# Kernel optimization log

Hardware: AMD Instinct MI355X
Metric: run time of the kernel (lower is better)

Reference implementation:

```python
import jax, jax.numpy as jnp
import numpy as np

EMBED_DIM = 768
NUM_HEADS = 12
HEAD_SIZE = EMBED_DIM // NUM_HEADS


def setup_inputs() -> dict:
    key = jax.random.key(0)
    ks = jax.random.split(key, 9)
    B, S, D = 4, 2048, EMBED_DIM
    scale = 1.0 / np.sqrt(D)
    x = jax.random.normal(ks[0], (B, S, D), dtype=jnp.float32)
    # Linear params (torch nn.Linear: y = x @ W.T + b); store W as [in, out] for einsum
    Wq = jax.random.normal(ks[1], (D, D), dtype=jnp.float32) * scale
    bq = jnp.zeros((D,), dtype=jnp.float32)
    Wk = jax.random.normal(ks[2], (D, D), dtype=jnp.float32) * scale
    bk = jnp.zeros((D,), dtype=jnp.float32)
    Wv = jax.random.normal(ks[3], (D, D), dtype=jnp.float32) * scale
    bv = jnp.zeros((D,), dtype=jnp.float32)
    Wo = jax.random.normal(ks[4], (D, D), dtype=jnp.float32) * scale
    bo = jnp.zeros((D,), dtype=jnp.float32)
    return {"x": x, "Wq": Wq, "bq": bq, "Wk": Wk, "bk": bk,
            "Wv": Wv, "bv": bv, "Wo": Wo, "bo": bo}


def reference(x, Wq, bq, Wk, bk, Wv, bv, Wo, bo):
    B, S, D = x.shape
    H, hs = NUM_HEADS, HEAD_SIZE
    scale = hs ** (-0.5)
    # Projections
    Q = (x @ Wq + bq).reshape(B, S, H, hs)
    K = (x @ Wk + bk).reshape(B, S, H, hs)
    V = (x @ Wv + bv).reshape(B, S, H, hs)
    # Batched attention over all heads (equivalent to the per-head loop:
    # torch view splits last dim into H contiguous chunks; concat of per-head
    # outputs along -1 restores the same layout)
    scores = jnp.einsum('bqhd,bkhd->bhqk', Q, K) * scale  # [B,H,S,S]
    attn = jax.nn.softmax(scores, axis=-1)
    out = jnp.einsum('bhqk,bkhd->bqhd', attn, V).reshape(B, S, D)
    # Output projection; dropout is identity in eval mode
    return out @ Wo + bo
```

## Files before the change

kernel.cpp:

```cpp
#include <hip/hip_runtime.h>

typedef unsigned short ushort_t;
typedef __bf16 bf16x8 __attribute__((ext_vector_type(8)));
typedef float floatx4 __attribute__((ext_vector_type(4)));

__device__ inline ushort_t f2bf(float f) {
    __bf16 h = (__bf16)f;
    return __builtin_bit_cast(ushort_t, h);
}

__device__ inline void gload16(const void* g, void* l) {
    __builtin_amdgcn_global_load_lds((const __attribute__((address_space(1))) void*)g,
                                     (__attribute__((address_space(3))) void*)l, 16, 0, 0);
}

__global__ __launch_bounds__(256) void prep_kernel(
    const float* __restrict__ x, ushort_t* __restrict__ xbf,
    const float* __restrict__ W0, const float* __restrict__ W1,
    const float* __restrict__ W2, const float* __restrict__ W3,
    ushort_t* __restrict__ T0, ushort_t* __restrict__ T1,
    ushort_t* __restrict__ T2, ushort_t* __restrict__ T3) {
    int bx = blockIdx.x;
    int tid = threadIdx.x;
    if (bx < 2304) {
        __shared__ float t[32][33];
        int w = bx / 576, rem = bx % 576;
        const float* W; ushort_t* T;
        switch (w) {
            case 0: W = W0; T = T0; break;
            case 1: W = W1; T = T1; break;
            case 2: W = W2; T = T2; break;
            default: W = W3; T = T3; break;
        }
        int n0 = (rem / 24) * 32, k0 = (rem % 24) * 32;
        int tx = tid & 31, ty = tid >> 5;
        for (int i = 0; i < 4; ++i)
            t[ty + i * 8][tx] = W[(k0 + ty + i * 8) * 768 + n0 + tx];
        __syncthreads();
        for (int i = 0; i < 4; ++i)
            T[(n0 + ty + i * 8) * 768 + k0 + tx] = f2bf(t[tx][ty + i * 8]);
    } else {
        int i = ((bx - 2304) * 256 + tid) * 4;
        float4 v = *(const float4*)(x + i);
        ushort4 u;
        u.x = f2bf(v.x); u.y = f2bf(v.y); u.z = f2bf(v.z); u.w = f2bf(v.w);
        *(ushort4*)(xbf + i) = u;
    }
}

__global__ __launch_bounds__(256) void gemm_qkv(
    const ushort_t* __restrict__ A,
    const ushort_t* __restrict__ Tq, const ushort_t* __restrict__ Tk, const ushort_t* __restrict__ Tv,
    const float* __restrict__ bq, const float* __restrict__ bk, const float* __restrict__ bv,
    ushort_t* __restrict__ Qb, ushort_t* __restrict__ Kb, ushort_t* __restrict__ Vtb) {
    __shared__ ushort_t As[128 * 64];
    __shared__ ushort_t Bs[64 * 64];
    int tid = threadIdx.x;
    int m0 = blockIdx.x * 128;
    int by = blockIdx.y;
    int which = by / 12;
    int n0 = (by % 12) * 64;
    const ushort_t* Bt = which == 0 ? Tq : (which == 1 ? Tk : Tv);
    const float* bias = which == 0 ? bq : (which == 1 ? bk : bv);

    int wave = tid >> 6;
    int lane = tid & 63;
    int ln = tid & 15;
    int quad = (tid >> 4) & 3;
    int wm = wave * 32;
    int lr = lane >> 3;
    int lc = (lane & 7) * 8;

    floatx4 acc[2][4];
    floatx4 z = {0.f, 0.f, 0.f, 0.f};
    for (int i = 0; i < 2; ++i)
        for (int j = 0; j < 4; ++j) acc[i][j] = z;

    for (int kt = 0; kt < 12; ++kt) {
        int k0 = kt * 64;
        __syncthreads();
        for (int i = 0; i < 4; ++i) {
            int c = wave * 4 + i;
            gload16(&A[(m0 + c * 8 + lr) * 768 + k0 + lc], &As[c * 512]);
        }
        for (int i = 0; i < 2; ++i) {
            int c = wave * 2 + i;
            gload16(&Bt[(n0 + c * 8 + lr) * 768 + k0 + lc], &Bs[c * 512]);
        }
        __syncthreads();
        for (int ks = 0; ks < 2; ++ks) {
            bf16x8 a[2], b[4];
            for (int i = 0; i < 2; ++i)
                a[i] = *(const bf16x8*)&As[(wm + i * 16 + ln) * 64 + ks * 32 + quad * 8];
            for (int j = 0; j < 4; ++j)
                b[j] = *(const bf16x8*)&Bs[(j * 16 + ln) * 64 + ks * 32 + quad * 8];
            for (int i = 0; i < 2; ++i)
                for (int j = 0; j < 4; ++j)
                    acc[i][j] = __builtin_amdgcn_mfma_f32_16x16x32_bf16(a[i], b[j], acc[i][j], 0, 0, 0);
        }
    }

    const float QSCALE = 0.125f * 1.44269504088896f;
    for (int i = 0; i < 2; ++i) {
        for (int j = 0; j < 4; ++j) {
            int gn = n0 + j * 16 + ln;
            float bia = bias[gn];
            int h = gn >> 6, dd = gn & 63;
            for (int r = 0; r < 4; ++r) {
                int gm = m0 + wm + i * 16 + quad * 4 + r;
                int bb = gm >> 11, ss = gm & 2047;
                float v = acc[i][j][r] + bia;
                if (which == 0) {
                    Qb[((bb * 12 + h) * 2048 + ss) * 64 + dd] = f2bf(v * QSCALE);
                } else if (which == 1) {
                    Kb[((bb * 12 + h) * 2048 + ss) * 64 + dd] = f2bf(v);
                } else {
                    Vtb[((bb * 12 + h) * 64 + dd) * 2048 + ss] = f2bf(v);
                }
            }
        }
    }
}

__global__ __launch_bounds__(256) void attn_kernel(
    const ushort_t* __restrict__ Qb, const ushort_t* __restrict__ Kb,
    const ushort_t* __restrict__ Vtb, ushort_t* __restrict__ Ob) {
    __shared__ ushort_t Ks[2][64 * 72];
    __shared__ ushort_t Vs[2][64 * 72];
    int tid = threadIdx.x;
    int qt = blockIdx.x;
    int bh = blockIdx.y;
    int wave = tid >> 6;
    int ln = tid & 15;
    int quad = (tid >> 4) & 3;
    int q0 = qt * 128 + wave * 32;

    const ushort_t* Qp = Qb + (size_t)bh * 2048 * 64;
    const ushort_t* Kp = Kb + (size_t)bh * 2048 * 64;
    const ushort_t* Vp = Vtb + (size_t)bh * 64 * 2048;

    bf16x8 bqf[2][2];
    for (int g = 0; g < 2; ++g)
        for (int ks = 0; ks < 2; ++ks)
            bqf[g][ks] = *(const bf16x8*)&Qp[(q0 + g * 16 + ln) * 64 + ks * 32 + quad * 8];

    int srow = tid >> 3;
    int c8 = tid & 7;
    int scol = c8 * 8;
    int u = c8 & 3;
    int vcol = (c8 >> 2) * 32 + (u & 1) * 16 + (u >> 1) * 4;

    uint4 kreg[2], vreg[2];

    for (int p = 0; p < 2; ++p) {
        kreg[p] = *(const uint4*)&Kp[(p * 32 + srow) * 64 + scol];
        vreg[p] = *(const uint4*)&Vp[(p * 32 + srow) * 2048 + scol];
    }
    for (int p = 0; p < 2; ++p) {
        *(uint4*)&Ks[0][(p * 32 + srow) * 72 + scol] = kreg[p];
        ushort_t* vb = &Vs[0][(p * 32 + srow) * 72 + vcol];
        *(uint2*)vb = make_uint2(vreg[p].x, vreg[p].y);
        *(uint2*)(vb + 8) = make_uint2(vreg[p].z, vreg[p].w);
    }
    __syncthreads();

    floatx4 o_acc[2][4];
    float lsum[2] = {0.f, 0.f};
    floatx4 z = {0.f, 0.f, 0.f, 0.f};
    for (int g = 0; g < 2; ++g)
        for (int m4 = 0; m4 < 4; ++m4) o_acc[g][m4] = z;

    for (int kt = 0; kt < 32; ++kt) {
        int cur = kt & 1;
        if (kt < 31) {
            for (int p = 0; p < 2; ++p) {
                kreg[p] = *(const uint4*)&Kp[((kt + 1) * 64 + p * 32 + srow) * 64 + scol];
                vreg[p] = *(const uint4*)&Vp[(p * 32 + srow) * 2048 + (kt + 1) * 64 + scol];
            }
        }

        const ushort_t* KsH = Ks[cur];
        const ushort_t* VsH = Vs[cur];

        bf16x8 ak[4][2];
        for (int m4 = 0; m4 < 4; ++m4)
            for (int ks = 0; ks < 2; ++ks)
                ak[m4][ks] = *(const bf16x8*)&KsH[(m4 * 16 + ln) * 72 + ks * 32 + quad * 8];

        floatx4 st[2][4];
        for (int g = 0; g < 2; ++g)
            for (int m4 = 0; m4 < 4; ++m4) {
                floatx4 s = z;
                s = __builtin_amdgcn_mfma_f32_16x16x32_bf16(ak[m4][0], bqf[g][0], s, 0, 0, 0);
                s = __builtin_amdgcn_mfma_f32_16x16x32_bf16(ak[m4][1], bqf[g][1], s, 0, 0, 0);
                st[g][m4] = s;
            }

        float pv[2][4][4];
        for (int g = 0; g < 2; ++g)
            for (int m4 = 0; m4 < 4; ++m4)
                for (int r = 0; r < 4; ++r) {
                    float e = __builtin_amdgcn_exp2f(st[g][m4][r]);
                    pv[g][m4][r] = e;
                    lsum[g] += e;
                }

        bf16x8 av[4][2];
        for (int m4 = 0; m4 < 4; ++m4)
            for (int c = 0; c < 2; ++c)
                av[m4][c] = *(const bf16x8*)&VsH[(m4 * 16 + ln) * 72 + c * 32 + quad * 8];

        for (int g = 0; g < 2; ++g) {
            bf16x8 bp[2];
            for (int c = 0; c < 2; ++c) {
                bf16x8 b;
                b[0] = (__bf16)pv[g][2 * c][0];
                b[1] = (__bf16)pv[g][2 * c][1];
                b[2] = (__bf16)pv[g][2 * c][2];
                b[3] = (__bf16)pv[g][2 * c][3];
                b[4] = (__bf16)pv[g][2 * c + 1][0];
                b[5] = (__bf16)pv[g][2 * c + 1][1];
                b[6] = (__bf16)pv[g][2 * c + 1][2];
                b[7] = (__bf16)pv[g][2 * c + 1][3];
                bp[c] = b;
            }
            for (int m4 = 0; m4 < 4; ++m4)
                for (int c = 0; c < 2; ++c)
                    o_acc[g][m4] = __builtin_amdgcn_mfma_f32_16x16x32_bf16(av[m4][c], bp[c], o_acc[g][m4], 0, 0, 0);
        }

        if (kt < 31) {
            int nxt = cur ^ 1;
            for (int p = 0; p < 2; ++p) {
                *(uint4*)&Ks[nxt][(p * 32 + srow) * 72 + scol] = kreg[p];
                ushort_t* vb = &Vs[nxt][(p * 32 + srow) * 72 + vcol];
                *(uint2*)vb = make_uint2(vreg[p].x, vreg[p].y);
                *(uint2*)(vb + 8) = make_uint2(vreg[p].z, vreg[p].w);
            }
        }
        __syncthreads();
    }

    for (int g = 0; g < 2; ++g) {
        lsum[g] += __shfl_xor(lsum[g], 16);
        lsum[g] += __shfl_xor(lsum[g], 32);
    }

    int b = bh / 12, h = bh % 12;
    for (int g = 0; g < 2; ++g) {
        float inv = 1.f / lsum[g];
        int token = b * 2048 + q0 + g * 16 + ln;
        for (int m4 = 0; m4 < 4; ++m4)
            for (int r = 0; r < 4; ++r)
                Ob[token * 768 + h * 64 + m4 * 16 + quad * 4 + r] = f2bf(o_acc[g][m4][r] * inv);
    }
}

__global__ __launch_bounds__(256) void gemm_out(
    const ushort_t* __restrict__ A, const ushort_t* __restrict__ Bt,
    const float* __restrict__ bias, float* __restrict__ out) {
    __shared__ ushort_t As[64 * 64];
    __shared__ ushort_t Bs[64 * 64];
    int tid = threadIdx.x;
    int m0 = blockIdx.x * 64;
    int n0 = blockIdx.y * 64;

    int wave = tid >> 6;
    int lane = tid & 63;
    int ln = tid & 15;
    int quad = (tid >> 4) & 3;
    int lr = lane >> 3;
    int lc = (lane & 7) * 8;

    floatx4 acc[4];
    floatx4 z = {0.f, 0.f, 0.f, 0.f};
    for (int i = 0; i < 4; ++i) acc[i] = z;

    for (int kt = 0; kt < 12; ++kt) {
        int k0 = kt * 64;
        __syncthreads();
        for (int i = 0; i < 2; ++i) {
            int c = wave * 2 + i;
            gload16(&A[(m0 + c * 8 + lr) * 768 + k0 + lc], &As[c * 512]);
            gload16(&Bt[(n0 + c * 8 + lr) * 768 + k0 + lc], &Bs[c * 512]);
        }
        __syncthreads();
        for (int ks = 0; ks < 2; ++ks) {
            bf16x8 b = *(const bf16x8*)&Bs[(wave * 16 + ln) * 64 + ks * 32 + quad * 8];
            for (int i = 0; i < 4; ++i) {
                bf16x8 a = *(const bf16x8*)&As[(i * 16 + ln) * 64 + ks * 32 + quad * 8];
                acc[i] = __builtin_amdgcn_mfma_f32_16x16x32_bf16(a, b, acc[i], 0, 0, 0);
            }
        }
    }

    int gn = n0 + wave * 16 + ln;
    float bia = bias[gn];
    for (int i = 0; i < 4; ++i) {
        for (int r = 0; r < 4; ++r) {
            int gm = m0 + i * 16 + quad * 4 + r;
            out[gm * 768 + gn] = acc[i][r] + bia;
        }
    }
}

extern "C" void kernel_launch(void* const* d_in, const int* in_sizes, int n_in,
                              void* d_out, int out_size, void* d_ws, size_t ws_size,
                              hipStream_t stream) {
    const float* x  = (const float*)d_in[0];
    const float* Wq = (const float*)d_in[1];
    const float* bq = (const float*)d_in[2];
    const float* Wk = (const float*)d_in[3];
    const float* bk = (const float*)d_in[4];
    const float* Wv = (const float*)d_in[5];
    const float* bv = (const float*)d_in[6];
    const float* Wo = (const float*)d_in[7];
    const float* bo = (const float*)d_in[8];

    const int NTOK = 4 * 2048;
    const int NELT = NTOK * 768;
    const int WELT = 768 * 768;

    ushort_t* xbf = (ushort_t*)d_ws;
    ushort_t* Tq  = xbf + NELT;
    ushort_t* Tk  = Tq + WELT;
    ushort_t* Tv  = Tk + WELT;
    ushort_t* To  = Tv + WELT;
    ushort_t* Qb  = To + WELT;
    ushort_t* Kb  = Qb + NELT;
    ushort_t* Vtb = Kb + NELT;
    ushort_t* Ob  = Vtb + NELT;

    prep_kernel<<<8448, 256, 0, stream>>>(x, xbf, Wq, Wk, Wv, Wo, Tq, Tk, Tv, To);
    gemm_qkv<<<dim3(64, 36), 256, 0, stream>>>(xbf, Tq, Tk, Tv, bq, bk, bv, Qb, Kb, Vtb);
    attn_kernel<<<dim3(16, 48), 256, 0, stream>>>(Qb, Kb, Vtb, Ob);
    gemm_out<<<dim3(128, 12), 256, 0, stream>>>(Ob, To, bo, (float*)d_out);
}
```

Before: 232.2 us.

## Stage V transpose through LDS and compute softmax row sums with MFMA

The V projection epilogue now writes its tile transposed into shared memory and then emits coalesced 16-byte stores to the transposed V buffer, instead of scattered 2-byte strided global stores. In the attention kernel, the per-row exponential sum is computed by an extra MFMA against a vector of ones using the bf16-rounded probabilities, replacing scalar adds and cross-lane shuffles. This removes VALU work and keeps the normaliser consistent with the bf16 P used for PV, at the cost of two extra MFMAs per tile per group and an added barrier plus LDS round trip in the V epilogue.

```diff
diff --git a/kernel.cpp b/kernel.cpp
--- a/kernel.cpp
+++ b/kernel.cpp
@@ -53,8 +53,9 @@
     const ushort_t* __restrict__ Tq, const ushort_t* __restrict__ Tk, const ushort_t* __restrict__ Tv,
     const float* __restrict__ bq, const float* __restrict__ bk, const float* __restrict__ bv,
     ushort_t* __restrict__ Qb, ushort_t* __restrict__ Kb, ushort_t* __restrict__ Vtb) {
-    __shared__ ushort_t As[128 * 64];
-    __shared__ ushort_t Bs[64 * 64];
+    __shared__ ushort_t sh[128 * 64 + 64 * 64];
+    ushort_t* As = sh;
+    ushort_t* Bs = sh + 128 * 64;
     int tid = threadIdx.x;
     int m0 = blockIdx.x * 128;
     int by = blockIdx.y;
@@ -101,23 +102,47 @@
     }
 
     const float QSCALE = 0.125f * 1.44269504088896f;
-    for (int i = 0; i < 2; ++i) {
+    if (which != 2) {
+        for (int i = 0; i < 2; ++i) {
+            for (int j = 0; j < 4; ++j) {
+                int gn = n0 + j * 16 + ln;
+                float bia = bias[gn];
+                int h = gn >> 6, dd = gn & 63;
+                for (int r = 0; r < 4; ++r) {
+                    int gm = m0 + wm + i * 16 + quad * 4 + r;
+                    int bb = gm >> 11, ss = gm & 2047;
+                    float v = acc[i][j][r] + bia;
+                    if (which == 0) {
+                        Qb[((bb * 12 + h) * 2048 + ss) * 64 + dd] = f2bf(v * QSCALE);
+                    } else {
+                        Kb[((bb * 12 + h) * 2048 + ss) * 64 + dd] = f2bf(v);
+                    }
+                }
+            }
+        }
+    } else {
+        __syncthreads();
+        ushort_t* tr = sh;
         for (int j = 0; j < 4; ++j) {
-            int gn = n0 + j * 16 + ln;
-            float bia = bias[gn];
-            int h = gn >> 6, dd = gn & 63;
-            for (int r = 0; r < 4; ++r) {
-                int gm = m0 + wm + i * 16 + quad * 4 + r;
-                int bb = gm >> 11, ss = gm & 2047;
-                float v = acc[i][j][r] + bia;
-                if (which == 0) {
-                    Qb[((bb * 12 + h) * 2048 + ss) * 64 + dd] = f2bf(v * QSCALE);
-                } else if (which == 1) {
-                    Kb[((bb * 12 + h) * 2048 + ss) * 64 + dd] = f2bf(v);
-                } else {
-                    Vtb[((bb * 12 + h) * 64 + dd) * 2048 + ss] = f2bf(v);
-                }
-            }
+            int nl = j * 16 + ln;
+            float bia = bias[n0 + nl];
+            for (int i = 0; i < 2; ++i) {
+                ushort4 u;
+                u.x = f2bf(acc[i][j][0] + bia);
+                u.y = f2bf(acc[i][j][1] + bia);
+                u.z = f2bf(acc[i][j][2] + bia);
+                u.w = f2bf(acc[i][j][3] + bia);
+                *(ushort4*)&tr[nl * 136 + wm + i * 16 + quad * 4] = u;
+            }
+        }
+        __syncthreads();
+        int bb = m0 >> 11, ss0 = m0 & 2047;
+        int head = by % 12;
+        for (int p = 0; p < 4; ++p) {
+            int n = p * 16 + (tid >> 4);
+            int mc = (tid & 15) * 8;
+            uint4 v = *(const uint4*)&tr[n * 136 + mc];
+            *(uint4*)&Vtb[(size_t)((bb * 12 + head) * 64 + n) * 2048 + ss0 + mc] = v;
         }
     }
 }
@@ -144,6 +169,9 @@
         for (int ks = 0; ks < 2; ++ks)
             bqf[g][ks] = *(const bf16x8*)&Qp[(q0 + g * 16 + ln) * 64 + ks * 32 + quad * 8];
 
+    bf16x8 ones;
+    for (int k = 0; k < 8; ++k) ones[k] = (__bf16)1.0f;
+
     int srow = tid >> 3;
     int c8 = tid & 7;
     int scol = c8 * 8;
@@ -165,10 +193,12 @@
     __syncthreads();
 
     floatx4 o_acc[2][4];
-    float lsum[2] = {0.f, 0.f};
+    floatx4 s_acc[2];
     floatx4 z = {0.f, 0.f, 0.f, 0.f};
-    for (int g = 0; g < 2; ++g)
+    for (int g = 0; g < 2; ++g) {
+        s_acc[g] = z;
         for (int m4 = 0; m4 < 4; ++m4) o_acc[g][m4] = z;
+    }
 
     for (int kt = 0; kt < 32; ++kt) {
         int cur = kt & 1;
@@ -199,11 +229,8 @@
         float pv[2][4][4];
         for (int g = 0; g < 2; ++g)
             for (int m4 = 0; m4 < 4; ++m4)
-                for (int r = 0; r < 4; ++r) {
-                    float e = __builtin_amdgcn_exp2f(st[g][m4][r]);
-                    pv[g][m4][r] = e;
-                    lsum[g] += e;
-                }
+                for (int r = 0; r < 4; ++r)
+                    pv[g][m4][r] = __builtin_amdgcn_exp2f(st[g][m4][r]);
 
         bf16x8 av[4][2];
         for (int m4 = 0; m4 < 4; ++m4)
@@ -227,6 +254,8 @@
             for (int m4 = 0; m4 < 4; ++m4)
                 for (int c = 0; c < 2; ++c)
                     o_acc[g][m4] = __builtin_amdgcn_mfma_f32_16x16x32_bf16(av[m4][c], bp[c], o_acc[g][m4], 0, 0, 0);
+            for (int c = 0; c < 2; ++c)
+                s_acc[g] = __builtin_amdgcn_mfma_f32_16x16x32_bf16(ones, bp[c], s_acc[g], 0, 0, 0);
         }
 
         if (kt < 31) {
@@ -241,14 +270,9 @@
         __syncthreads();
     }
 
-    for (int g = 0; g < 2; ++g) {
-        lsum[g] += __shfl_xor(lsum[g], 16);
-        lsum[g] += __shfl_xor(lsum[g], 32);
-    }
-
     int b = bh / 12, h = bh % 12;
     for (int g = 0; g < 2; ++g) {
-        float inv = 1.f / lsum[g];
+        float inv = 1.f / s_acc[g][0];
         int token = b * 2048 + q0 + g * 16 + ln;
         for (int m4 = 0; m4 < 4; ++m4)
             for (int r = 0; r < 4; ++r)
```

After: 235.6 us. Within noise of the previous version (+1.5%).
